# Optimization experiments

Measured on AMD Instinct MI355X. Metric: run time of the kernel, lower is better.

The kernel has to match this reference:

```python
import jax, jax.numpy as jnp
import numpy as np

N_NODES = 50000
N_EDGES = 800000
IN_C, HID, OUT_C = 128, 128, 16
N_GRAPHS = 128


def setup_inputs() -> dict:
    key = jax.random.key(0)
    ks = jax.random.split(key, 8)
    x = jax.random.normal(ks[0], (N_NODES, IN_C), dtype=jnp.float32)
    edge_index = jax.random.randint(ks[1], (2, N_EDGES), 0, N_NODES, dtype=jnp.int64)
    batch = jnp.sort(jax.random.randint(ks[2], (N_NODES,), 0, N_GRAPHS, dtype=jnp.int64))
    s1 = 1.0 / np.sqrt(IN_C)
    s2 = 1.0 / np.sqrt(HID)
    W1 = jax.random.normal(ks[3], (IN_C, HID), dtype=jnp.float32) * s1
    b1 = jnp.zeros((HID,), dtype=jnp.float32)
    W2 = jax.random.normal(ks[4], (HID, HID), dtype=jnp.float32) * s2
    b2 = jnp.zeros((HID,), dtype=jnp.float32)
    Wfc = jax.random.normal(ks[5], (HID, OUT_C), dtype=jnp.float32) * s2
    bfc = jnp.zeros((OUT_C,), dtype=jnp.float32)
    return {"x": x, "edge_index": edge_index, "batch": batch,
            "W1": W1, "b1": b1, "W2": W2, "b2": b2, "Wfc": Wfc, "bfc": bfc}


def _gcn_conv(x, W, b, src, dst, deg_inv_sqrt, n_nodes):
    # linear transform first (PyG order), then normalized sparse aggregation
    h = x @ W  # [N, H]
    norm = deg_inv_sqrt[src] * deg_inv_sqrt[dst]  # [E+N] (self-loops appended)
    msgs = h[src] * norm[:, None]  # [E+N, H] dominant gather
    agg = jax.ops.segment_sum(msgs, dst, num_segments=n_nodes)
    return agg + b


def reference(x, edge_index, batch, W1, b1, W2, b2, Wfc, bfc):
    n = x.shape[0]
    loops = jnp.arange(n, dtype=edge_index.dtype)
    src = jnp.concatenate([edge_index[0], loops])
    dst = jnp.concatenate([edge_index[1], loops])
    # symmetric normalization with self-loops: deg computed on dst
    deg = jax.ops.segment_sum(jnp.ones_like(src, dtype=x.dtype), dst, num_segments=n)
    deg_inv_sqrt = jnp.where(deg > 0, jax.lax.rsqrt(jnp.maximum(deg, 1.0)), 0.0)

    h = jax.nn.relu(_gcn_conv(x, W1, b1, src, dst, deg_inv_sqrt, n))
    h = jax.nn.relu(_gcn_conv(h, W2, b2, src, dst, deg_inv_sqrt, n))

    # global mean pool over graph ids
    sums = jax.ops.segment_sum(h, batch, num_segments=N_GRAPHS)
    counts = jax.ops.segment_sum(jnp.ones((n,), dtype=h.dtype), batch, num_segments=N_GRAPHS)
    pooled = sums / jnp.maximum(counts, 1.0)[:, None]  # [G, H]

    logits = pooled @ Wfc + bfc  # [G, OUT_C]
    return jax.nn.log_softmax(logits, axis=1)
```

## Files before the change

kernel.cpp:

```cpp
#include <hip/hip_runtime.h>

#define N_NODES  50000
#define N_EDGES  800000
#define HID      128
#define OUT_C    16
#define N_GRAPHS 128
#define MAXDEG   64
#define NSLICE   6250
#define EPB      1024
#define FILLB    6256
#define GEMMB    782
#define AGB      3125
#define PAD      136

typedef __attribute__((ext_vector_type(8))) short bf16x8;
typedef __attribute__((ext_vector_type(4))) float f32x4;
typedef __attribute__((ext_vector_type(8))) unsigned short us8;
typedef __attribute__((ext_vector_type(4))) unsigned short us4;

__device__ __forceinline__ unsigned short f2bf(float f) {
  unsigned u = __float_as_uint(f);
  u += 0x7fffu + ((u >> 16) & 1u);
  return (unsigned short)(u >> 16);
}

__device__ __forceinline__ void gemm_compute_store(
    unsigned short* sA, const float* __restrict__ W,
    unsigned short* __restrict__ T, int base) {
  const int tid = threadIdx.x;
  const int lane = tid & 63;
  const int w = tid >> 6;
  const int l15 = lane & 15;
  const int quad = lane >> 4;
  __syncthreads();

  f32x4 acc[4][2];
#pragma unroll
  for (int nt = 0; nt < 4; ++nt)
#pragma unroll
    for (int c = 0; c < 2; ++c) acc[nt][c] = (f32x4)(0.f);

  const int ct0 = w * 2;
  const int ncol = ct0 * 16 + l15;
#pragma unroll
  for (int ks = 0; ks < 4; ++ks) {
    const int koff = ks * 32 + quad * 8;
    bf16x8 a[4], bfr[2];
#pragma unroll
    for (int c = 0; c < 2; ++c) {
      const float* wp = W + (size_t)koff * HID + ncol + c * 16;
#pragma unroll
      for (int j = 0; j < 8; ++j) bfr[c][j] = (short)f2bf(wp[(size_t)j * HID]);
    }
#pragma unroll
    for (int nt = 0; nt < 4; ++nt)
      a[nt] = *(const bf16x8*)(sA + (nt * 16 + l15) * PAD + koff);
#pragma unroll
    for (int nt = 0; nt < 4; ++nt)
#pragma unroll
      for (int c = 0; c < 2; ++c)
        acc[nt][c] = __builtin_amdgcn_mfma_f32_16x16x32_bf16(a[nt], bfr[c], acc[nt][c], 0, 0, 0);
  }
  __syncthreads();

#pragma unroll
  for (int nt = 0; nt < 4; ++nt)
#pragma unroll
    for (int c = 0; c < 2; ++c)
#pragma unroll
      for (int r = 0; r < 4; ++r)
        sA[(nt * 16 + quad * 4 + r) * PAD + (ct0 + c) * 16 + l15] = f2bf(acc[nt][c][r]);
  __syncthreads();
#pragma unroll
  for (int i = 0; i < 4; ++i) {
    int idx = tid + i * 256;
    int nrow = idx >> 4;
    int col = (idx & 15) * 8;
    int node = base + nrow;
    if (node < N_NODES)
      *(us8*)(T + (size_t)node * HID + col) = *(const us8*)(sA + nrow * PAD + col);
  }
}

__device__ __forceinline__ void stage_a_f32(unsigned short* sA,
                                            const float* __restrict__ H, int base) {
#pragma unroll
  for (int i = 0; i < 8; ++i) {
    int idx = threadIdx.x + i * 256;
    int nrow = idx >> 5;
    int c4 = (idx & 31) * 4;
    float4 v = make_float4(0.f, 0.f, 0.f, 0.f);
    int node = base + nrow;
    if (node < N_NODES) v = *(const float4*)(H + (size_t)node * HID + c4);
    us4 b;
    b.x = f2bf(v.x); b.y = f2bf(v.y); b.z = f2bf(v.z); b.w = f2bf(v.w);
    *(us4*)(sA + nrow * PAD + c4) = b;
  }
}

__global__ __launch_bounds__(256) void mega_kernel(
    const int* __restrict__ src, const int* __restrict__ dst,
    int* __restrict__ deg, unsigned short* __restrict__ ell,
    const int* __restrict__ batch, int* __restrict__ start,
    const float* __restrict__ x, const float* __restrict__ W1,
    unsigned short* __restrict__ T) {
  __shared__ unsigned short sA[64 * PAD];
  int b = blockIdx.x;
  if (b < FILLB) {
    const int slice = b & 7;
    const int e0 = (b >> 3) * EPB;
    const int e1 = min(e0 + EPB, N_EDGES);
    const unsigned lo = slice * NSLICE;
    for (int e = e0 + threadIdx.x; e < e1; e += 256) {
      int d = __builtin_nontemporal_load(dst + e);
      if ((unsigned)(d - lo) < (unsigned)NSLICE) {
        int p = atomicAdd(&deg[d], 1);
        if (p < MAXDEG) ell[(d << 6) + p] = (unsigned short)src[e];
      }
    }
  } else if (b == FILLB) {
    int t = threadIdx.x;
    if (t <= N_GRAPHS) {
      int lo = 0, hi = N_NODES;
      while (lo < hi) {
        int mid = (lo + hi) >> 1;
        if (batch[mid] < t) lo = mid + 1; else hi = mid;
      }
      start[t] = lo;
    }
  } else {
    const int base = (b - FILLB - 1) * 64;
    stage_a_f32(sA, x, base);
    gemm_compute_store(sA, W1, T, base);
  }
}

__device__ __forceinline__ void agg_node_pack(
    int node, int lane, const unsigned int* __restrict__ Tb,
    const unsigned short* __restrict__ ell, const int* __restrict__ deg,
    unsigned int* __restrict__ ellw,
    float bx, float by, float& ox, float& oy) {
  int dn = deg[node];
  float dd = rsqrtf((float)dn + 1.0f);
  unsigned sv = Tb[(size_t)node * 64 + lane];
  float wself = dd * dd;
  float ax = __int_as_float(sv << 16) * wself;
  float ay = __int_as_float(sv & 0xffff0000u) * wself;
  int m = min(dn, MAXDEG);
  int s0 = node << 6;
  int sidx = 0; float wv = 0.f;
  if (lane < m) {
    sidx = (int)ell[s0 + lane];
    wv = rsqrtf((float)deg[sidx] + 1.0f) * dd;
    unsigned short hw = __builtin_bit_cast(unsigned short, (_Float16)wv);
    ellw[s0 + lane] = (unsigned)sidx | ((unsigned)hw << 16);
  }
  int j = 0;
  for (; j + 8 <= m; j += 8) {
#pragma unroll
    for (int q = 0; q < 8; ++q) {
      int s = __builtin_amdgcn_readlane(sidx, j + q);
      float w = __int_as_float(__builtin_amdgcn_readlane(__float_as_int(wv), j + q));
      unsigned t = Tb[(size_t)s * 64 + lane];
      ax += w * __int_as_float(t << 16);
      ay += w * __int_as_float(t & 0xffff0000u);
    }
  }
  for (; j < m; ++j) {
    int s = __builtin_amdgcn_readlane(sidx, j);
    float w = __int_as_float(__builtin_amdgcn_readlane(__float_as_int(wv), j));
    unsigned t = Tb[(size_t)s * 64 + lane];
    ax += w * __int_as_float(t << 16);
    ay += w * __int_as_float(t & 0xffff0000u);
  }
  ox = fmaxf(ax + bx, 0.f);
  oy = fmaxf(ay + by, 0.f);
}

__device__ __forceinline__ void agg_node_packed(
    int node, int lane, const unsigned int* __restrict__ Tb,
    const unsigned int* __restrict__ ellw, const int* __restrict__ deg,
    float bx, float by, float& ox, float& oy) {
  int dn = deg[node];
  float dd = rsqrtf((float)dn + 1.0f);
  unsigned sv = Tb[(size_t)node * 64 + lane];
  float wself = dd * dd;
  float ax = __int_as_float(sv << 16) * wself;
  float ay = __int_as_float(sv & 0xffff0000u) * wself;
  int m = min(dn, MAXDEG);
  unsigned pw = 0;
  if (lane < m) pw = ellw[(node << 6) + lane];
  int j = 0;
  for (; j + 8 <= m; j += 8) {
#pragma unroll
    for (int q = 0; q < 8; ++q) {
      unsigned v = (unsigned)__builtin_amdgcn_readlane((int)pw, j + q);
      int s = (int)(v & 0xffffu);
      float w = (float)__builtin_bit_cast(_Float16, (unsigned short)(v >> 16));
      unsigned t = Tb[(size_t)s * 64 + lane];
      ax += w * __int_as_float(t << 16);
      ay += w * __int_as_float(t & 0xffff0000u);
    }
  }
  for (; j < m; ++j) {
    unsigned v = (unsigned)__builtin_amdgcn_readlane((int)pw, j);
    int s = (int)(v & 0xffffu);
    float w = (float)__builtin_bit_cast(_Float16, (unsigned short)(v >> 16));
    unsigned t = Tb[(size_t)s * 64 + lane];
    ax += w * __int_as_float(t << 16);
    ay += w * __int_as_float(t & 0xffff0000u);
  }
  ox = fmaxf(ax + bx, 0.f);
  oy = fmaxf(ay + by, 0.f);
}

__global__ __launch_bounds__(1024) void agg_gemm_kernel(
    const unsigned int* __restrict__ Tb, const unsigned short* __restrict__ ell,
    const int* __restrict__ deg, const float* __restrict__ bias,
    const float* __restrict__ W, unsigned int* __restrict__ ellw,
    unsigned short* __restrict__ T2) {
  __shared__ unsigned short sA[16 * PAD];
  const int tid = threadIdx.x;
  const int lane = tid & 63;
  const int w = tid >> 6;
  const int l15 = lane & 15;
  const int quad = lane >> 4;
  const int base = blockIdx.x * 16;

  {
    float2 b = ((const float2*)bias)[lane];
    float ox, oy;
    agg_node_pack(base + w, lane, Tb, ell, deg, ellw, b.x, b.y, ox, oy);
    *(unsigned*)(sA + w * PAD + lane * 2) =
        (unsigned)f2bf(ox) | ((unsigned)f2bf(oy) << 16);
  }
  __syncthreads();

  f32x4 acc = (f32x4)(0.f);
  if (w < 8) {
    const int ncol = w * 16 + l15;
#pragma unroll
    for (int ks = 0; ks < 4; ++ks) {
      const int koff = ks * 32 + quad * 8;
      bf16x8 a = *(const bf16x8*)(sA + l15 * PAD + koff);
      bf16x8 bfr;
      const float* wp = W + (size_t)koff * HID + ncol;
#pragma unroll
      for (int j = 0; j < 8; ++j) bfr[j] = (short)f2bf(wp[(size_t)j * HID]);
      acc = __builtin_amdgcn_mfma_f32_16x16x32_bf16(a, bfr, acc, 0, 0, 0);
    }
  }
  __syncthreads();
  if (w < 8) {
#pragma unroll
    for (int r = 0; r < 4; ++r)
      sA[(quad * 4 + r) * PAD + w * 16 + l15] = f2bf(acc[r]);
  }
  __syncthreads();
  if (tid < 256) {
    int nrow = tid >> 4;
    int col = (tid & 15) * 8;
    *(us8*)(T2 + (size_t)(base + nrow) * HID + col) = *(const us8*)(sA + nrow * PAD + col);
  }
}

__global__ __launch_bounds__(256) void aggregate_kernel(
    const unsigned int* __restrict__ Tb, const unsigned int* __restrict__ ellw,
    const int* __restrict__ deg, const float* __restrict__ bias,
    unsigned int* __restrict__ Hb) {
  int node = (blockIdx.x * blockDim.x + threadIdx.x) >> 6;
  int lane = threadIdx.x & 63;
  if (node >= N_NODES) return;
  float2 b = ((const float2*)bias)[lane];
  float ox, oy;
  agg_node_packed(node, lane, Tb, ellw, deg, b.x, b.y, ox, oy);
  Hb[(size_t)node * 64 + lane] =
      (unsigned)f2bf(ox) | ((unsigned)f2bf(oy) << 16);
}

__global__ __launch_bounds__(256) void pool_partial_kernel(
    const unsigned int* __restrict__ Hb, const int* __restrict__ start,
    float* __restrict__ pooled) {
  __shared__ float2 red[4][64];
  int g = blockIdx.x >> 2;
  int chunk = blockIdx.x & 3;
  int n0 = start[g], n1 = start[g + 1];
  int lane = threadIdx.x & 63, w = threadIdx.x >> 6;
  float ax = 0.f, ay = 0.f;
  for (int n = n0 + chunk * 4 + w; n < n1; n += 16) {
    unsigned h = Hb[(size_t)n * 64 + lane];
    ax += __int_as_float(h << 16);
    ay += __int_as_float(h & 0xffff0000u);
  }
  red[w][lane] = make_float2(ax, ay);
  __syncthreads();
  if (threadIdx.x < 64) {
    float2 a = red[0][lane], b = red[1][lane], c = red[2][lane], d = red[3][lane];
    atomicAdd(&pooled[g * HID + lane * 2],     a.x + b.x + c.x + d.x);
    atomicAdd(&pooled[g * HID + lane * 2 + 1], a.y + b.y + c.y + d.y);
  }
}

__global__ __launch_bounds__(64) void head_kernel(
    const float* __restrict__ pooled, const int* __restrict__ start,
    const float* __restrict__ Wfc, const float* __restrict__ bfc,
    float* __restrict__ out) {
  int g = blockIdx.x;
  int lane = threadIdx.x;
  int o = lane & 15;
  float inv = 1.0f / fmaxf((float)(start[g + 1] - start[g]), 1.0f);
  float part = 0.f;
  for (int k = (lane >> 4); k < HID; k += 4)
    part += pooled[g * HID + k] * inv * Wfc[k * OUT_C + o];
  part += __shfl_xor(part, 16);
  part += __shfl_xor(part, 32);
  float logit = part + bfc[o];
  float m = logit;
#pragma unroll
  for (int d = 8; d >= 1; d >>= 1) m = fmaxf(m, __shfl_xor(m, d, 16));
  float e = __expf(logit - m);
  float s = e;
#pragma unroll
  for (int d = 8; d >= 1; d >>= 1) s += __shfl_xor(s, d, 16);
  float r = logit - m - __logf(s);
  if (lane < 16) out[g * OUT_C + o] = r;
}

extern "C" void kernel_launch(void* const* d_in, const int* in_sizes, int n_in,
                              void* d_out, int out_size, void* d_ws, size_t ws_size,
                              hipStream_t stream) {
  const float* x    = (const float*)d_in[0];
  const int*   ei   = (const int*)d_in[1];
  const int*   batch= (const int*)d_in[2];
  const float* W1   = (const float*)d_in[3];
  const float* b1   = (const float*)d_in[4];
  const float* W2   = (const float*)d_in[5];
  const float* b2   = (const float*)d_in[6];
  const float* Wfc  = (const float*)d_in[7];
  const float* bfc  = (const float*)d_in[8];
  float* out = (float*)d_out;
  const int* src = ei;
  const int* dst = ei + N_EDGES;

  char* p = (char*)d_ws;
  auto alloc = [&](size_t bytes) { char* r = p; p += (bytes + 255) & ~255ull; return r; };
  int*   degI   = (int*)alloc((size_t)N_NODES * 4);
  float* pooled = (float*)alloc((size_t)N_GRAPHS * HID * 4);
  int*   start  = (int*)alloc((N_GRAPHS + 1) * 4);
  unsigned short* ell = (unsigned short*)alloc((size_t)N_NODES * MAXDEG * 2);
  unsigned int*   ellw= (unsigned int*)alloc((size_t)N_NODES * MAXDEG * 4);
  unsigned short* T   = (unsigned short*)alloc((size_t)N_NODES * HID * 2);
  unsigned short* T2  = (unsigned short*)alloc((size_t)N_NODES * HID * 2);
  unsigned short* Hb  = (unsigned short*)alloc((size_t)N_NODES * HID * 2);

  hipMemsetAsync(degI, 0, ((size_t)N_NODES * 4 + 255 & ~255ull) +
                          (size_t)N_GRAPHS * HID * 4, stream);

  int agg_blocks = (N_NODES * 64 + 255) / 256;

  mega_kernel<<<FILLB + 1 + GEMMB, 256, 0, stream>>>(src, dst, degI, ell,
                                                     batch, start, x, W1, T);
  agg_gemm_kernel<<<AGB, 1024, 0, stream>>>((const unsigned int*)T, ell, degI,
                                            b1, W2, ellw, T2);
  aggregate_kernel<<<agg_blocks, 256, 0, stream>>>((const unsigned int*)T2, ellw, degI, b2,
                                                   (unsigned int*)Hb);
  pool_partial_kernel<<<N_GRAPHS * 4, 256, 0, stream>>>((const unsigned int*)Hb, start,
                                                        pooled);
  head_kernel<<<N_GRAPHS, 64, 0, stream>>>(pooled, start, Wfc, bfc, out);
}
```

Measured before the change: 231.5 us.

## Interleave fill and GEMM blocks, pad gather loops, process two nodes per wave

```diff
diff --git a/kernel.cpp b/kernel.cpp
--- a/kernel.cpp
+++ b/kernel.cpp
@@ -106,19 +106,26 @@
     unsigned short* __restrict__ T) {
   __shared__ unsigned short sA[64 * PAD];
   int b = blockIdx.x;
-  if (b < FILLB) {
-    const int slice = b & 7;
-    const int e0 = (b >> 3) * EPB;
-    const int e1 = min(e0 + EPB, N_EDGES);
-    const unsigned lo = slice * NSLICE;
-    for (int e = e0 + threadIdx.x; e < e1; e += 256) {
-      int d = __builtin_nontemporal_load(dst + e);
-      if ((unsigned)(d - lo) < (unsigned)NSLICE) {
-        int p = atomicAdd(&deg[d], 1);
-        if (p < MAXDEG) ell[(d << 6) + p] = (unsigned short)src[e];
+  if (b < FILLB + GEMMB) {
+    if (b % 9 == 8) {
+      const int base = (b / 9) * 64;
+      stage_a_f32(sA, x, base);
+      gemm_compute_store(sA, W1, T, base);
+    } else {
+      const int fi = b - (b + 1) / 9;
+      const int slice = fi & 7;
+      const int e0 = (fi >> 3) * EPB;
+      const int e1 = min(e0 + EPB, N_EDGES);
+      const unsigned lo = slice * NSLICE;
+      for (int e = e0 + threadIdx.x; e < e1; e += 256) {
+        int d = __builtin_nontemporal_load(dst + e);
+        if ((unsigned)(d - lo) < (unsigned)NSLICE) {
+          int p = atomicAdd(&deg[d], 1);
+          if (p < MAXDEG) ell[(d << 6) + p] = (unsigned short)src[e];
+        }
       }
     }
-  } else if (b == FILLB) {
+  } else {
     int t = threadIdx.x;
     if (t <= N_GRAPHS) {
       int lo = 0, hi = N_NODES;
@@ -128,10 +135,6 @@
       }
       start[t] = lo;
     }
-  } else {
-    const int base = (b - FILLB - 1) * 64;
-    stage_a_f32(sA, x, base);
-    gemm_compute_store(sA, W1, T, base);
   }
 }
 
@@ -155,8 +158,8 @@
     unsigned short hw = __builtin_bit_cast(unsigned short, (_Float16)wv);
     ellw[s0 + lane] = (unsigned)sidx | ((unsigned)hw << 16);
   }
-  int j = 0;
-  for (; j + 8 <= m; j += 8) {
+  const int mt = (m + 7) & ~7;
+  for (int j = 0; j < mt; j += 8) {
 #pragma unroll
     for (int q = 0; q < 8; ++q) {
       int s = __builtin_amdgcn_readlane(sidx, j + q);
@@ -165,50 +168,6 @@
       ax += w * __int_as_float(t << 16);
       ay += w * __int_as_float(t & 0xffff0000u);
     }
-  }
-  for (; j < m; ++j) {
-    int s = __builtin_amdgcn_readlane(sidx, j);
-    float w = __int_as_float(__builtin_amdgcn_readlane(__float_as_int(wv), j));
-    unsigned t = Tb[(size_t)s * 64 + lane];
-    ax += w * __int_as_float(t << 16);
-    ay += w * __int_as_float(t & 0xffff0000u);
-  }
-  ox = fmaxf(ax + bx, 0.f);
-  oy = fmaxf(ay + by, 0.f);
-}
-
-__device__ __forceinline__ void agg_node_packed(
-    int node, int lane, const unsigned int* __restrict__ Tb,
-    const unsigned int* __restrict__ ellw, const int* __restrict__ deg,
-    float bx, float by, float& ox, float& oy) {
-  int dn = deg[node];
-  float dd = rsqrtf((float)dn + 1.0f);
-  unsigned sv = Tb[(size_t)node * 64 + lane];
-  float wself = dd * dd;
-  float ax = __int_as_float(sv << 16) * wself;
-  float ay = __int_as_float(sv & 0xffff0000u) * wself;
-  int m = min(dn, MAXDEG);
-  unsigned pw = 0;
-  if (lane < m) pw = ellw[(node << 6) + lane];
-  int j = 0;
-  for (; j + 8 <= m; j += 8) {
-#pragma unroll
-    for (int q = 0; q < 8; ++q) {
-      unsigned v = (unsigned)__builtin_amdgcn_readlane((int)pw, j + q);
-      int s = (int)(v & 0xffffu);
-      float w = (float)__builtin_bit_cast(_Float16, (unsigned short)(v >> 16));
-      unsigned t = Tb[(size_t)s * 64 + lane];
-      ax += w * __int_as_float(t << 16);
-      ay += w * __int_as_float(t & 0xffff0000u);
-    }
-  }
-  for (; j < m; ++j) {
-    unsigned v = (unsigned)__builtin_amdgcn_readlane((int)pw, j);
-    int s = (int)(v & 0xffffu);
-    float w = (float)__builtin_bit_cast(_Float16, (unsigned short)(v >> 16));
-    unsigned t = Tb[(size_t)s * 64 + lane];
-    ax += w * __int_as_float(t << 16);
-    ay += w * __int_as_float(t & 0xffff0000u);
   }
   ox = fmaxf(ax + bx, 0.f);
   oy = fmaxf(ay + by, 0.f);
@@ -268,14 +227,46 @@
     const unsigned int* __restrict__ Tb, const unsigned int* __restrict__ ellw,
     const int* __restrict__ deg, const float* __restrict__ bias,
     unsigned int* __restrict__ Hb) {
-  int node = (blockIdx.x * blockDim.x + threadIdx.x) >> 6;
+  int wid = (blockIdx.x * 256 + threadIdx.x) >> 6;
   int lane = threadIdx.x & 63;
-  if (node >= N_NODES) return;
+  int n0 = wid * 2;
+  if (n0 >= N_NODES) return;
+  int n1 = n0 + 1;
   float2 b = ((const float2*)bias)[lane];
-  float ox, oy;
-  agg_node_packed(node, lane, Tb, ellw, deg, b.x, b.y, ox, oy);
-  Hb[(size_t)node * 64 + lane] =
-      (unsigned)f2bf(ox) | ((unsigned)f2bf(oy) << 16);
+  int d0 = deg[n0], d1 = deg[n1];
+  float r0 = rsqrtf((float)d0 + 1.f), r1 = rsqrtf((float)d1 + 1.f);
+  unsigned sv0 = Tb[(size_t)n0 * 64 + lane];
+  unsigned sv1 = Tb[(size_t)n1 * 64 + lane];
+  float ax0 = __int_as_float(sv0 << 16) * (r0 * r0);
+  float ay0 = __int_as_float(sv0 & 0xffff0000u) * (r0 * r0);
+  float ax1 = __int_as_float(sv1 << 16) * (r1 * r1);
+  float ay1 = __int_as_float(sv1 & 0xffff0000u) * (r1 * r1);
+  int m0 = min(d0, MAXDEG), m1 = min(d1, MAXDEG);
+  unsigned pw0 = 0, pw1 = 0;
+  if (lane < m0) pw0 = ellw[(n0 << 6) + lane];
+  if (lane < m1) pw1 = ellw[(n1 << 6) + lane];
+  const int mt = (max(m0, m1) + 7) & ~7;
+  for (int j = 0; j < mt; j += 8) {
+#pragma unroll
+    for (int q = 0; q < 8; ++q) {
+      unsigned v0 = (unsigned)__builtin_amdgcn_readlane((int)pw0, j + q);
+      unsigned v1 = (unsigned)__builtin_amdgcn_readlane((int)pw1, j + q);
+      unsigned t0 = Tb[(size_t)(v0 & 0xffffu) * 64 + lane];
+      unsigned t1 = Tb[(size_t)(v1 & 0xffffu) * 64 + lane];
+      float w0 = (float)__builtin_bit_cast(_Float16, (unsigned short)(v0 >> 16));
+      float w1 = (float)__builtin_bit_cast(_Float16, (unsigned short)(v1 >> 16));
+      ax0 += w0 * __int_as_float(t0 << 16);
+      ay0 += w0 * __int_as_float(t0 & 0xffff0000u);
+      ax1 += w1 * __int_as_float(t1 << 16);
+      ay1 += w1 * __int_as_float(t1 & 0xffff0000u);
+    }
+  }
+  Hb[(size_t)n0 * 64 + lane] =
+      (unsigned)f2bf(fmaxf(ax0 + b.x, 0.f)) |
+      ((unsigned)f2bf(fmaxf(ay0 + b.y, 0.f)) << 16);
+  Hb[(size_t)n1 * 64 + lane] =
+      (unsigned)f2bf(fmaxf(ax1 + b.x, 0.f)) |
+      ((unsigned)f2bf(fmaxf(ay1 + b.y, 0.f)) << 16);
 }
 
 __global__ __launch_bounds__(256) void pool_partial_kernel(
@@ -356,9 +347,9 @@
   hipMemsetAsync(degI, 0, ((size_t)N_NODES * 4 + 255 & ~255ull) +
                           (size_t)N_GRAPHS * HID * 4, stream);
 
-  int agg_blocks = (N_NODES * 64 + 255) / 256;
-
-  mega_kernel<<<FILLB + 1 + GEMMB, 256, 0, stream>>>(src, dst, degI, ell,
+  int agg_blocks = (N_NODES / 2 * 64 + 255) / 256;
+
+  mega_kernel<<<FILLB + GEMMB + 1, 256, 0, stream>>>(src, dst, degI, ell,
                                                      batch, start, x, W1, T);
   agg_gemm_kernel<<<AGB, 1024, 0, stream>>>((const unsigned int*)T, ell, degI,
                                             b1, W2, ellw, T2);
```

New measurement: 237.6 us. 1.03x slower.
